# Kernel tuning notes

Measured on AMD Instinct MI355X. Metric: run time of the kernel, lower is better.

## Reference

```python
import jax, jax.numpy as jnp
import numpy as np

VOCAB = 32000
D_MODEL = 1024
PATCH_LEN = 16
NHEAD = 8
B = 8
S = 4096


def setup_inputs() -> dict:
    key = jax.random.key(0)
    ks = jax.random.split(key, 8)
    token_inputs = jax.random.randint(ks[0], (B, S), 0, VOCAB, dtype=jnp.int64 if jax.config.jax_enable_x64 else jnp.int32)
    attention_mask = jax.random.randint(ks[1], (B, S), 0, 2).astype(bool)
    emb_weight = jax.random.normal(ks[2], (VOCAB, D_MODEL), dtype=jnp.float32) * 0.02
    patch_query = jax.random.normal(ks[3], (1, 1, D_MODEL), dtype=jnp.float32) * 0.02
    # nn.MultiheadAttention packed in-projection [3D, D] and out projection [D, D]
    lim = 1.0 / np.sqrt(D_MODEL)
    in_proj_w = jax.random.uniform(ks[4], (3 * D_MODEL, D_MODEL), jnp.float32, -lim, lim)
    in_proj_b = jnp.zeros((3 * D_MODEL,), jnp.float32)
    out_w = jax.random.uniform(ks[5], (D_MODEL, D_MODEL), jnp.float32, -lim, lim)
    out_b = jnp.zeros((D_MODEL,), jnp.float32)
    return {
        "token_inputs": token_inputs,
        "attention_mask": attention_mask,
        "emb_weight": emb_weight,
        "patch_query": patch_query,
        "in_proj_w": in_proj_w,
        "in_proj_b": in_proj_b,
        "out_w": out_w,
        "out_b": out_b,
    }


def reference(token_inputs, attention_mask, emb_weight, patch_query, in_proj_w, in_proj_b, out_w, out_b):
    d_model = emb_weight.shape[1]
    h, dh = NHEAD, d_model // NHEAD
    L = PATCH_LEN

    tok_emb = emb_weight[token_inputs]              # [B, S, D]
    bsz, seqlen, _ = tok_emb.shape
    # seqlen chosen divisible by PATCH_LEN -> pad_len == 0 (matches torch path)
    num_patches = seqlen // L
    BP = bsz * num_patches
    patch_tokens = tok_emb.reshape(BP, L, d_model)  # [BP, L, D]
    patch_mask = attention_mask.reshape(BP, L)      # True = valid token

    patch_valid = patch_mask.any(axis=1)            # [BP]
    # force position 0 valid for fully-empty patches (safe softmax)
    safe_mask = patch_mask | ((~patch_valid)[:, None] & (jnp.arange(L) == 0)[None, :])

    wq, wk, wv = jnp.split(in_proj_w, 3, axis=0)    # each [D, D]
    bq, bk, bv = jnp.split(in_proj_b, 3, axis=0)

    q = patch_query[0, 0] @ wq.T + bq               # [D] (same query for all patches)
    k = patch_tokens @ wk.T + bk                    # [BP, L, D]
    v = patch_tokens @ wv.T + bv                    # [BP, L, D]

    qh = q.reshape(h, dh)                           # [H, dh]
    kh = k.reshape(BP, L, h, dh)                    # [BP, L, H, dh]
    vh = v.reshape(BP, L, h, dh)

    scale = 1.0 / jnp.sqrt(jnp.asarray(dh, q.dtype))
    scores = jnp.einsum('hd,blhd->bhl', qh, kh) * scale   # [BP, H, L]
    scores = jnp.where(safe_mask[:, None, :], scores, -jnp.inf)
    attn = jax.nn.softmax(scores, axis=-1)                # [BP, H, L]

    ctx = jnp.einsum('bhl,blhd->bhd', attn, vh).reshape(BP, d_model)
    patch_latent = ctx @ out_w.T + out_b                  # [BP, D]

    patch_latent = patch_latent.reshape(bsz, num_patches, d_model)
    pv = patch_valid.reshape(bsz, num_patches)
    patch_latent = patch_latent * pv[..., None].astype(patch_latent.dtype)
    return patch_latent, pv
```

## Files before the change

### kernel.cpp

```cpp
#include <hip/hip_runtime.h>
#include <stdint.h>

#define OUT_LATENT (2048*1024)
#define SCALE 0.08838834764831845f

typedef float f32x4v __attribute__((ext_vector_type(4)));
typedef short s16x8  __attribute__((ext_vector_type(8)));

static __device__ inline unsigned short f2bf(float f) {
    union { float f; uint32_t u; } v; v.f = f;
    uint32_t u = v.u;
    return (unsigned short)((u + 0x7FFFu + ((u >> 16) & 1u)) >> 16);
}
static __device__ inline float bflo(uint32_t u) {
    union { uint32_t u; float f; } v; v.u = u << 16; return v.f;
}
static __device__ inline float bfhi(uint32_t u) {
    union { uint32_t u; float f; } v; v.u = u & 0xFFFF0000u; return v.f;
}

static __device__ __forceinline__ void async16(const unsigned short* g, unsigned short* l) {
    __builtin_amdgcn_global_load_lds(
        (const __attribute__((address_space(1))) void*)g,
        (__attribute__((address_space(3))) void*)l, 16, 0, 0);
}

__global__ __launch_bounds__(256) void k_prep(
    const float* __restrict__ ipw, const float* __restrict__ ipb,
    const float* __restrict__ pq, const float* __restrict__ ow,
    unsigned short* __restrict__ wv_dst, unsigned short* __restrict__ ow_dst,
    unsigned short* __restrict__ qkb, float* __restrict__ sb) {
    __shared__ float qs[128];
    __shared__ float part[128];
    int t = threadIdx.x, b = blockIdx.x;

    if (b < 2048) {
        const float* src; unsigned short* dst; int idx;
        if (b < 1024) { src = ipw + (size_t)2048 * 1024; dst = wv_dst; idx = b * 1024 + t * 4; }
        else          { src = ow;                        dst = ow_dst; idx = (b - 1024) * 1024 + t * 4; }
        float4 f = *(const float4*)(src + idx);
        ushort4 o; o.x = f2bf(f.x); o.y = f2bf(f.y); o.z = f2bf(f.z); o.w = f2bf(f.w);
        *(ushort4*)(dst + idx) = o;
        return;
    }

    int bb = b - 2048;
    int h = bb >> 3, jseg = bb & 7;

    {
        int dl = t >> 1, half = t & 1;
        const float* wrow = ipw + (size_t)(h * 128 + dl) * 1024 + half * 512;
        const float* pqh = pq + half * 512;
        float a = 0.f;
        #pragma unroll 8
        for (int j = 0; j < 512; j += 4) {
            float4 w = *(const float4*)(wrow + j);
            float4 p = *(const float4*)(pqh + j);
            a = fmaf(w.x, p.x, a); a = fmaf(w.y, p.y, a);
            a = fmaf(w.z, p.z, a); a = fmaf(w.w, p.w, a);
        }
        a += __shfl_xor(a, 1);
        if (!half) qs[dl] = a + ipb[h * 128 + dl];
    }
    __syncthreads();

    int jl = t & 127, dh = t >> 7;
    float acc = 0.f;
    const float* wbase = ipw + (size_t)(1024 + h * 128 + dh * 64) * 1024 + jseg * 128 + jl;
    #pragma unroll 8
    for (int d = 0; d < 64; ++d)
        acc = fmaf(qs[dh * 64 + d], wbase[(size_t)d * 1024], acc);
    if (dh) part[jl] = acc;
    __syncthreads();
    if (!dh) qkb[h * 1024 + jseg * 128 + jl] = f2bf((acc + part[jl]) * SCALE);
    if (jseg == 0 && t < 64) {
        const float* bk = ipb + 1024 + h * 128;
        float p = qs[t] * bk[t] + qs[t + 64] * bk[t + 64];
        #pragma unroll
        for (int m = 32; m >= 1; m >>= 1) p += __shfl_xor(p, m);
        if (t == 0) sb[h] = p * SCALE;
    }
}

__global__ __launch_bounds__(256) void k_attn(
    const int* __restrict__ tok_ids, const int* __restrict__ amask,
    const float* __restrict__ emb, const unsigned short* __restrict__ qkb,
    const float* __restrict__ sb, unsigned short* __restrict__ Mout,
    float* __restrict__ pv) {
    __shared__ unsigned short tokL[16][1032];
    __shared__ float scoresP[4][16][8];
    __shared__ float attnL[16][8];
    __shared__ int allzL;

    int bp = blockIdx.x, t = threadIdx.x;
    int wave = t >> 6, lane = t & 63, lrow = lane & 15, quad = lane >> 4;

    s16x8 bfr[8];
    {
        const unsigned short* qbase = qkb + (lane & 7) * 1024 + wave * 256 + quad * 8;
        #pragma unroll
        for (int s = 0; s < 8; ++s) bfr[s] = *(const s16x8*)(qbase + s * 32);
    }

    {
        int row = t >> 4, c = t & 15;
        int tid = tok_ids[bp * 16 + row];
        const float* erow = emb + (size_t)tid * 1024;
        #pragma unroll
        for (int i = 0; i < 16; ++i) {
            int j4 = c + i * 16;
            float4 f = *(const float4*)(erow + j4 * 4);
            ushort4 o; o.x = f2bf(f.x); o.y = f2bf(f.y); o.z = f2bf(f.z); o.w = f2bf(f.w);
            *(ushort4*)(&tokL[row][j4 * 4]) = o;
        }
    }
    if (t < 16) {
        int any = (amask[bp * 16 + t] != 0);
        any |= __shfl_xor(any, 1); any |= __shfl_xor(any, 2);
        any |= __shfl_xor(any, 4); any |= __shfl_xor(any, 8);
        if (t == 0) { pv[bp] = any ? 1.f : 0.f; allzL = any ? 0 : 1; }
    }
    __syncthreads();

    {
        f32x4v acc = (f32x4v){0.f, 0.f, 0.f, 0.f};
        const unsigned short* arow = &tokL[lrow][wave * 256 + quad * 8];
        #pragma unroll
        for (int s = 0; s < 8; ++s) {
            s16x8 af = *(const s16x8*)(arow + s * 32);
            acc = __builtin_amdgcn_mfma_f32_16x16x32_bf16(af, bfr[s], acc, 0, 0, 0);
        }
        if (lrow < 8) {
            #pragma unroll
            for (int r = 0; r < 4; ++r) scoresP[wave][quad * 4 + r][lrow] = acc[r];
        }
    }
    __syncthreads();

    if (t < 128) {
        int hh = t >> 4, ll = t & 15;
        float s = scoresP[0][ll][hh] + scoresP[1][ll][hh]
                + scoresP[2][ll][hh] + scoresP[3][ll][hh] + sb[hh];
        bool valid = (amask[bp * 16 + ll] != 0) || (allzL && ll == 0);
        s = valid ? s : -1e30f;
        float mx = s;
        mx = fmaxf(mx, __shfl_xor(mx, 1)); mx = fmaxf(mx, __shfl_xor(mx, 2));
        mx = fmaxf(mx, __shfl_xor(mx, 4)); mx = fmaxf(mx, __shfl_xor(mx, 8));
        float e = __expf(s - mx);
        float sum = e;
        sum += __shfl_xor(sum, 1); sum += __shfl_xor(sum, 2);
        sum += __shfl_xor(sum, 4); sum += __shfl_xor(sum, 8);
        attnL[ll][hh] = e / sum;
    }
    __syncthreads();

    float macc[8][4];
    #pragma unroll
    for (int h = 0; h < 8; ++h)
        #pragma unroll
        for (int c = 0; c < 4; ++c) macc[h][c] = 0.f;
    #pragma unroll
    for (int ll = 0; ll < 16; ++ll) {
        uint2 tv = *(const uint2*)(&tokL[ll][t * 4]);
        float t0 = bflo(tv.x), t1 = bfhi(tv.x), t2 = bflo(tv.y), t3 = bfhi(tv.y);
        float4 a0 = *(const float4*)(&attnL[ll][0]);
        float4 a1 = *(const float4*)(&attnL[ll][4]);
        macc[0][0] = fmaf(a0.x, t0, macc[0][0]); macc[0][1] = fmaf(a0.x, t1, macc[0][1]);
        macc[0][2] = fmaf(a0.x, t2, macc[0][2]); macc[0][3] = fmaf(a0.x, t3, macc[0][3]);
        macc[1][0] = fmaf(a0.y, t0, macc[1][0]); macc[1][1] = fmaf(a0.y, t1, macc[1][1]);
        macc[1][2] = fmaf(a0.y, t2, macc[1][2]); macc[1][3] = fmaf(a0.y, t3, macc[1][3]);
        macc[2][0] = fmaf(a0.z, t0, macc[2][0]); macc[2][1] = fmaf(a0.z, t1, macc[2][1]);
        macc[2][2] = fmaf(a0.z, t2, macc[2][2]); macc[2][3] = fmaf(a0.z, t3, macc[2][3]);
        macc[3][0] = fmaf(a0.w, t0, macc[3][0]); macc[3][1] = fmaf(a0.w, t1, macc[3][1]);
        macc[3][2] = fmaf(a0.w, t2, macc[3][2]); macc[3][3] = fmaf(a0.w, t3, macc[3][3]);
        macc[4][0] = fmaf(a1.x, t0, macc[4][0]); macc[4][1] = fmaf(a1.x, t1, macc[4][1]);
        macc[4][2] = fmaf(a1.x, t2, macc[4][2]); macc[4][3] = fmaf(a1.x, t3, macc[4][3]);
        macc[5][0] = fmaf(a1.y, t0, macc[5][0]); macc[5][1] = fmaf(a1.y, t1, macc[5][1]);
        macc[5][2] = fmaf(a1.y, t2, macc[5][2]); macc[5][3] = fmaf(a1.y, t3, macc[5][3]);
        macc[6][0] = fmaf(a1.z, t0, macc[6][0]); macc[6][1] = fmaf(a1.z, t1, macc[6][1]);
        macc[6][2] = fmaf(a1.z, t2, macc[6][2]); macc[6][3] = fmaf(a1.z, t3, macc[6][3]);
        macc[7][0] = fmaf(a1.w, t0, macc[7][0]); macc[7][1] = fmaf(a1.w, t1, macc[7][1]);
        macc[7][2] = fmaf(a1.w, t2, macc[7][2]); macc[7][3] = fmaf(a1.w, t3, macc[7][3]);
    }
    #pragma unroll
    for (int h = 0; h < 8; ++h) {
        ushort4 o;
        o.x = f2bf(macc[h][0]); o.y = f2bf(macc[h][1]);
        o.z = f2bf(macc[h][2]); o.w = f2bf(macc[h][3]);
        *(ushort4*)(Mout + ((size_t)(h * 2048 + bp)) * 1024 + t * 4) = o;
    }
}

__device__ __forceinline__ void gemm64x128_dbuf(
    const unsigned short* __restrict__ A, const unsigned short* __restrict__ B,
    unsigned short* As, unsigned short* Bs, f32x4v acc[4][2]) {
    int t = threadIdx.x;
    int wave = t >> 6, lane = t & 63, lrow = lane & 15, quad = lane >> 4;
    int r4 = t >> 2, seg = (t & 3) * 8;
    #pragma unroll
    for (int mi = 0; mi < 4; ++mi)
        #pragma unroll
        for (int ni = 0; ni < 2; ++ni) acc[mi][ni] = (f32x4v){0.f, 0.f, 0.f, 0.f};
    async16(A + (size_t)r4 * 1024 + seg,        As + t * 8);
    async16(B + (size_t)r4 * 1024 + seg,        Bs + t * 8);
    async16(B + (size_t)(r4 + 64) * 1024 + seg, Bs + (256 + t) * 8);
    for (int s = 0; s < 32; ++s) {
        __syncthreads();
        if (s < 31) {
            int nk = (s + 1) * 32;
            int pb = (s + 1) & 1;
            async16(A + (size_t)r4 * 1024 + nk + seg,        As + pb * 2048 + t * 8);
            async16(B + (size_t)r4 * 1024 + nk + seg,        Bs + pb * 4096 + t * 8);
            async16(B + (size_t)(r4 + 64) * 1024 + nk + seg, Bs + pb * 4096 + (256 + t) * 8);
        }
        const unsigned short* Asc = As + (s & 1) * 2048;
        const unsigned short* Bsc = Bs + (s & 1) * 4096;
        s16x8 af[4], bf[2];
        #pragma unroll
        for (int mi = 0; mi < 4; ++mi)
            af[mi] = *(const s16x8*)(Asc + (mi * 16 + lrow) * 32 + quad * 8);
        #pragma unroll
        for (int ni = 0; ni < 2; ++ni)
            bf[ni] = *(const s16x8*)(Bsc + (wave * 32 + ni * 16 + lrow) * 32 + quad * 8);
        #pragma unroll
        for (int mi = 0; mi < 4; ++mi)
            #pragma unroll
            for (int ni = 0; ni < 2; ++ni)
                acc[mi][ni] = __builtin_amdgcn_mfma_f32_16x16x32_bf16(af[mi], bf[ni], acc[mi][ni], 0, 0, 0);
    }
}

__global__ __launch_bounds__(256) void k_gemm_ctx(
    const unsigned short* __restrict__ M, const unsigned short* __restrict__ wv,
    const float* __restrict__ ipb, unsigned short* __restrict__ ctx) {
    __shared__ unsigned short As[2 * 2048], Bs[2 * 4096];
    int mb = blockIdx.x, h = blockIdx.y;
    f32x4v acc[4][2];
    gemm64x128_dbuf(M + ((size_t)h * 2048 + mb * 64) * 1024,
                    wv + (size_t)h * 128 * 1024, As, Bs, acc);
    int t = threadIdx.x, wave = t >> 6, lane = t & 63, lrow = lane & 15, quad = lane >> 4;
    #pragma unroll
    for (int ni = 0; ni < 2; ++ni) {
        int n_g = h * 128 + wave * 32 + ni * 16 + lrow;
        float bias = ipb[2048 + n_g];
        #pragma unroll
        for (int mi = 0; mi < 4; ++mi) {
            #pragma unroll
            for (int r = 0; r < 4; ++r) {
                int m_g = mb * 64 + mi * 16 + quad * 4 + r;
                ctx[(size_t)m_g * 1024 + n_g] = f2bf(acc[mi][ni][r] + bias);
            }
        }
    }
}

__global__ __launch_bounds__(256) void k_gemm_out(
    const unsigned short* __restrict__ ctx, const unsigned short* __restrict__ ow,
    const float* __restrict__ outb, const float* __restrict__ pv,
    float* __restrict__ out) {
    __shared__ unsigned short As[2 * 2048], Bs[2 * 4096];
    int mb = blockIdx.x, nb = blockIdx.y;
    f32x4v acc[4][2];
    gemm64x128_dbuf(ctx + (size_t)mb * 64 * 1024,
                    ow + (size_t)nb * 128 * 1024, As, Bs, acc);
    int t = threadIdx.x, wave = t >> 6, lane = t & 63, lrow = lane & 15, quad = lane >> 4;
    #pragma unroll
    for (int ni = 0; ni < 2; ++ni) {
        int n_g = nb * 128 + wave * 32 + ni * 16 + lrow;
        float bias = outb[n_g];
        #pragma unroll
        for (int mi = 0; mi < 4; ++mi) {
            #pragma unroll
            for (int r = 0; r < 4; ++r) {
                int m_g = mb * 64 + mi * 16 + quad * 4 + r;
                out[(size_t)m_g * 1024 + n_g] = (acc[mi][ni][r] + bias) * pv[m_g];
            }
        }
    }
    if (nb == 0 && t < 64) out[OUT_LATENT + mb * 64 + t] = pv[mb * 64 + t];
}

extern "C" void kernel_launch(void* const* d_in, const int* in_sizes, int n_in,
                              void* d_out, int out_size, void* d_ws, size_t ws_size,
                              hipStream_t stream) {
    const int*   tok = (const int*)d_in[0];
    const int*   msk = (const int*)d_in[1];
    const float* emb = (const float*)d_in[2];
    const float* pq  = (const float*)d_in[3];
    const float* ipw = (const float*)d_in[4];
    const float* ipb = (const float*)d_in[5];
    const float* ow  = (const float*)d_in[6];
    const float* ob  = (const float*)d_in[7];
    float* out = (float*)d_out;
    char* ws = (char*)d_ws;

    float*          sb_f  = (float*)(ws + 4096);
    float*          pv_f  = (float*)(ws + 8192);
    unsigned short* qk_b  = (unsigned short*)(ws + 16384);
    unsigned short* wv_b  = (unsigned short*)(ws + 32768);
    unsigned short* ow_b  = (unsigned short*)(ws + 32768 + 2097152);
    unsigned short* ctx_b = (unsigned short*)(ws + 32768 + 2 * 2097152);
    unsigned short* M_b   = (unsigned short*)(ws + 32768 + 2 * 2097152 + 4194304);

    k_prep<<<dim3(2112), dim3(256), 0, stream>>>(ipw, ipb, pq, ow, wv_b, ow_b, qk_b, sb_f);
    k_attn<<<dim3(2048), dim3(256), 0, stream>>>(tok, msk, emb, qk_b, sb_f, M_b, pv_f);
    k_gemm_ctx<<<dim3(32, 8), dim3(256), 0, stream>>>(M_b, wv_b, ipb, ctx_b);
    k_gemm_out<<<dim3(32, 8), dim3(256), 0, stream>>>(ctx_b, ow_b, ob, pv_f, out);
}
```

Before: 300.6 us.

## Fuse all stages into a persistent megakernel with dependency counters

Replaces the four kernel launches with one persistent kernel where blocks pull work tickets from an atomic counter. Per-stage completion counters let the ctx and out GEMM tiles for one 128-row group start as soon as that group's attention and weight conversion finish, so stages overlap instead of serialising. GEMM tiles change from a double-buffered 64x128 tile to a single-buffered 128x64 tile, and shared memory becomes a union across roles. This adds spin-wait latency, per-step sync stalls from dropping double buffering, and a memset launch, and it relies on ticket order to avoid deadlock.

```diff
diff --git a/kernel.cpp b/kernel.cpp
--- a/kernel.cpp
+++ b/kernel.cpp
@@ -1,16 +1,23 @@
 #include <hip/hip_runtime.h>
 #include <stdint.h>
 
+typedef unsigned int u32;
+typedef unsigned short u16;
+
 #define OUT_LATENT (2048*1024)
 #define SCALE 0.08838834764831845f
 
 typedef float f32x4v __attribute__((ext_vector_type(4)));
 typedef short s16x8  __attribute__((ext_vector_type(8)));
 
-static __device__ inline unsigned short f2bf(float f) {
+#define T_CONV0 64
+#define T_G0    2112
+#define T_END   4672
+
+static __device__ inline u16 f2bf(float f) {
     union { float f; uint32_t u; } v; v.f = f;
     uint32_t u = v.u;
-    return (unsigned short)((u + 0x7FFFu + ((u >> 16) & 1u)) >> 16);
+    return (u16)((u + 0x7FFFu + ((u >> 16) & 1u)) >> 16);
 }
 static __device__ inline float bflo(uint32_t u) {
     union { uint32_t u; float f; } v; v.u = u << 16; return v.f;
@@ -18,35 +25,37 @@
 static __device__ inline float bfhi(uint32_t u) {
     union { uint32_t u; float f; } v; v.u = u & 0xFFFF0000u; return v.f;
 }
-
-static __device__ __forceinline__ void async16(const unsigned short* g, unsigned short* l) {
+static __device__ __forceinline__ void async16(const u16* g, u16* l) {
     __builtin_amdgcn_global_load_lds(
         (const __attribute__((address_space(1))) void*)g,
         (__attribute__((address_space(3))) void*)l, 16, 0, 0);
 }
 
-__global__ __launch_bounds__(256) void k_prep(
+union SMem {
+    struct { u16 tokL[16][1032]; float scoresP[4][16][8]; float attnL[16][8]; int allz; } a;
+    struct { u16 As[128 * 32]; u16 Bs[64 * 32]; } g;
+    struct { float qs[128]; float part[128]; } q;
+};
+
+static __device__ __forceinline__ void wait_ge(u32* p, u32 need) {
+    if (threadIdx.x == 0) {
+        while (__hip_atomic_load(p, __ATOMIC_RELAXED, __HIP_MEMORY_SCOPE_AGENT) < need)
+            __builtin_amdgcn_s_sleep(32);
+        (void)__hip_atomic_load(p, __ATOMIC_ACQUIRE, __HIP_MEMORY_SCOPE_AGENT);
+    }
+    __syncthreads();
+}
+static __device__ __forceinline__ void done_add(u32* p) {
+    __syncthreads();
+    if (threadIdx.x == 0)
+        (void)__hip_atomic_fetch_add(p, 1u, __ATOMIC_RELEASE, __HIP_MEMORY_SCOPE_AGENT);
+}
+
+static __device__ void role_qk(SMem& sm, int tk,
     const float* __restrict__ ipw, const float* __restrict__ ipb,
-    const float* __restrict__ pq, const float* __restrict__ ow,
-    unsigned short* __restrict__ wv_dst, unsigned short* __restrict__ ow_dst,
-    unsigned short* __restrict__ qkb, float* __restrict__ sb) {
-    __shared__ float qs[128];
-    __shared__ float part[128];
-    int t = threadIdx.x, b = blockIdx.x;
-
-    if (b < 2048) {
-        const float* src; unsigned short* dst; int idx;
-        if (b < 1024) { src = ipw + (size_t)2048 * 1024; dst = wv_dst; idx = b * 1024 + t * 4; }
-        else          { src = ow;                        dst = ow_dst; idx = (b - 1024) * 1024 + t * 4; }
-        float4 f = *(const float4*)(src + idx);
-        ushort4 o; o.x = f2bf(f.x); o.y = f2bf(f.y); o.z = f2bf(f.z); o.w = f2bf(f.w);
-        *(ushort4*)(dst + idx) = o;
-        return;
-    }
-
-    int bb = b - 2048;
-    int h = bb >> 3, jseg = bb & 7;
-
+    const float* __restrict__ pq, u16* __restrict__ qkb, float* __restrict__ sb,
+    u32* ctr) {
+    int h = tk >> 3, jseg = tk & 7, t = threadIdx.x;
     {
         int dl = t >> 1, half = t & 1;
         const float* wrow = ipw + (size_t)(h * 128 + dl) * 1024 + half * 512;
@@ -60,48 +69,55 @@
             a = fmaf(w.z, p.z, a); a = fmaf(w.w, p.w, a);
         }
         a += __shfl_xor(a, 1);
-        if (!half) qs[dl] = a + ipb[h * 128 + dl];
-    }
-    __syncthreads();
-
+        if (!half) sm.q.qs[dl] = a + ipb[h * 128 + dl];
+    }
+    __syncthreads();
     int jl = t & 127, dh = t >> 7;
     float acc = 0.f;
     const float* wbase = ipw + (size_t)(1024 + h * 128 + dh * 64) * 1024 + jseg * 128 + jl;
     #pragma unroll 8
     for (int d = 0; d < 64; ++d)
-        acc = fmaf(qs[dh * 64 + d], wbase[(size_t)d * 1024], acc);
-    if (dh) part[jl] = acc;
-    __syncthreads();
-    if (!dh) qkb[h * 1024 + jseg * 128 + jl] = f2bf((acc + part[jl]) * SCALE);
+        acc = fmaf(sm.q.qs[dh * 64 + d], wbase[(size_t)d * 1024], acc);
+    if (dh) sm.q.part[jl] = acc;
+    __syncthreads();
+    if (!dh) qkb[h * 1024 + jseg * 128 + jl] = f2bf((acc + sm.q.part[jl]) * SCALE);
     if (jseg == 0 && t < 64) {
         const float* bk = ipb + 1024 + h * 128;
-        float p = qs[t] * bk[t] + qs[t + 64] * bk[t + 64];
+        float p = sm.q.qs[t] * bk[t] + sm.q.qs[t + 64] * bk[t + 64];
         #pragma unroll
         for (int m = 32; m >= 1; m >>= 1) p += __shfl_xor(p, m);
         if (t == 0) sb[h] = p * SCALE;
     }
-}
-
-__global__ __launch_bounds__(256) void k_attn(
+    done_add(ctr + 1);
+}
+
+static __device__ void role_conv(int b,
+    const float* __restrict__ ipw, const float* __restrict__ ow,
+    u16* __restrict__ wv_dst, u16* __restrict__ ow_dst, u32* ctr) {
+    int t = threadIdx.x;
+    const float* src; u16* dst; int idx;
+    if (b < 1024) { src = ipw + (size_t)2048 * 1024; dst = wv_dst; idx = b * 1024 + t * 4; }
+    else          { src = ow;                        dst = ow_dst; idx = (b - 1024) * 1024 + t * 4; }
+    float4 f = *(const float4*)(src + idx);
+    ushort4 o; o.x = f2bf(f.x); o.y = f2bf(f.y); o.z = f2bf(f.z); o.w = f2bf(f.w);
+    *(ushort4*)(dst + idx) = o;
+    done_add(ctr + (b < 1024 ? 2 : 3));
+}
+
+static __device__ void role_attn(SMem& sm, int bp,
     const int* __restrict__ tok_ids, const int* __restrict__ amask,
-    const float* __restrict__ emb, const unsigned short* __restrict__ qkb,
-    const float* __restrict__ sb, unsigned short* __restrict__ Mout,
-    float* __restrict__ pv) {
-    __shared__ unsigned short tokL[16][1032];
-    __shared__ float scoresP[4][16][8];
-    __shared__ float attnL[16][8];
-    __shared__ int allzL;
-
-    int bp = blockIdx.x, t = threadIdx.x;
+    const float* __restrict__ emb, const u16* __restrict__ qkb,
+    const float* __restrict__ sb, u16* __restrict__ Mout,
+    float* __restrict__ pv, u32* ctr) {
+    int t = threadIdx.x;
     int wave = t >> 6, lane = t & 63, lrow = lane & 15, quad = lane >> 4;
 
     s16x8 bfr[8];
     {
-        const unsigned short* qbase = qkb + (lane & 7) * 1024 + wave * 256 + quad * 8;
+        const u16* qbase = qkb + (lane & 7) * 1024 + wave * 256 + quad * 8;
         #pragma unroll
         for (int s = 0; s < 8; ++s) bfr[s] = *(const s16x8*)(qbase + s * 32);
     }
-
     {
         int row = t >> 4, c = t & 15;
         int tid = tok_ids[bp * 16 + row];
@@ -111,20 +127,20 @@
             int j4 = c + i * 16;
             float4 f = *(const float4*)(erow + j4 * 4);
             ushort4 o; o.x = f2bf(f.x); o.y = f2bf(f.y); o.z = f2bf(f.z); o.w = f2bf(f.w);
-            *(ushort4*)(&tokL[row][j4 * 4]) = o;
+            *(ushort4*)(&sm.a.tokL[row][j4 * 4]) = o;
         }
     }
     if (t < 16) {
         int any = (amask[bp * 16 + t] != 0);
         any |= __shfl_xor(any, 1); any |= __shfl_xor(any, 2);
         any |= __shfl_xor(any, 4); any |= __shfl_xor(any, 8);
-        if (t == 0) { pv[bp] = any ? 1.f : 0.f; allzL = any ? 0 : 1; }
+        if (t == 0) { pv[bp] = any ? 1.f : 0.f; sm.a.allz = any ? 0 : 1; }
     }
     __syncthreads();
 
     {
         f32x4v acc = (f32x4v){0.f, 0.f, 0.f, 0.f};
-        const unsigned short* arow = &tokL[lrow][wave * 256 + quad * 8];
+        const u16* arow = &sm.a.tokL[lrow][wave * 256 + quad * 8];
         #pragma unroll
         for (int s = 0; s < 8; ++s) {
             s16x8 af = *(const s16x8*)(arow + s * 32);
@@ -132,16 +148,16 @@
         }
         if (lrow < 8) {
             #pragma unroll
-            for (int r = 0; r < 4; ++r) scoresP[wave][quad * 4 + r][lrow] = acc[r];
+            for (int r = 0; r < 4; ++r) sm.a.scoresP[wave][quad * 4 + r][lrow] = acc[r];
         }
     }
     __syncthreads();
 
     if (t < 128) {
         int hh = t >> 4, ll = t & 15;
-        float s = scoresP[0][ll][hh] + scoresP[1][ll][hh]
-                + scoresP[2][ll][hh] + scoresP[3][ll][hh] + sb[hh];
-        bool valid = (amask[bp * 16 + ll] != 0) || (allzL && ll == 0);
+        float s = sm.a.scoresP[0][ll][hh] + sm.a.scoresP[1][ll][hh]
+                + sm.a.scoresP[2][ll][hh] + sm.a.scoresP[3][ll][hh] + sb[hh];
+        bool valid = (amask[bp * 16 + ll] != 0) || (sm.a.allz && ll == 0);
         s = valid ? s : -1e30f;
         float mx = s;
         mx = fmaxf(mx, __shfl_xor(mx, 1)); mx = fmaxf(mx, __shfl_xor(mx, 2));
@@ -150,7 +166,7 @@
         float sum = e;
         sum += __shfl_xor(sum, 1); sum += __shfl_xor(sum, 2);
         sum += __shfl_xor(sum, 4); sum += __shfl_xor(sum, 8);
-        attnL[ll][hh] = e / sum;
+        sm.a.attnL[ll][hh] = e / sum;
     }
     __syncthreads();
 
@@ -161,10 +177,10 @@
         for (int c = 0; c < 4; ++c) macc[h][c] = 0.f;
     #pragma unroll
     for (int ll = 0; ll < 16; ++ll) {
-        uint2 tv = *(const uint2*)(&tokL[ll][t * 4]);
+        uint2 tv = *(const uint2*)(&sm.a.tokL[ll][t * 4]);
         float t0 = bflo(tv.x), t1 = bfhi(tv.x), t2 = bflo(tv.y), t3 = bfhi(tv.y);
-        float4 a0 = *(const float4*)(&attnL[ll][0]);
-        float4 a1 = *(const float4*)(&attnL[ll][4]);
+        float4 a0 = *(const float4*)(&sm.a.attnL[ll][0]);
+        float4 a1 = *(const float4*)(&sm.a.attnL[ll][4]);
         macc[0][0] = fmaf(a0.x, t0, macc[0][0]); macc[0][1] = fmaf(a0.x, t1, macc[0][1]);
         macc[0][2] = fmaf(a0.x, t2, macc[0][2]); macc[0][3] = fmaf(a0.x, t3, macc[0][3]);
         macc[1][0] = fmaf(a0.y, t0, macc[1][0]); macc[1][1] = fmaf(a0.y, t1, macc[1][1]);
@@ -189,39 +205,35 @@
         o.z = f2bf(macc[h][2]); o.w = f2bf(macc[h][3]);
         *(ushort4*)(Mout + ((size_t)(h * 2048 + bp)) * 1024 + t * 4) = o;
     }
-}
-
-__device__ __forceinline__ void gemm64x128_dbuf(
-    const unsigned short* __restrict__ A, const unsigned short* __restrict__ B,
-    unsigned short* As, unsigned short* Bs, f32x4v acc[4][2]) {
+    done_add(ctr + 4 + (bp >> 7));
+}
+
+static __device__ __forceinline__ void gemm_tile_128x64(
+    const u16* __restrict__ A, const u16* __restrict__ B, SMem& sm,
+    f32x4v acc[4][2]) {
     int t = threadIdx.x;
     int wave = t >> 6, lane = t & 63, lrow = lane & 15, quad = lane >> 4;
+    int wm = wave & 1, wn = wave >> 1;
     int r4 = t >> 2, seg = (t & 3) * 8;
+    u16* As = sm.g.As; u16* Bs = sm.g.Bs;
     #pragma unroll
     for (int mi = 0; mi < 4; ++mi)
         #pragma unroll
         for (int ni = 0; ni < 2; ++ni) acc[mi][ni] = (f32x4v){0.f, 0.f, 0.f, 0.f};
-    async16(A + (size_t)r4 * 1024 + seg,        As + t * 8);
-    async16(B + (size_t)r4 * 1024 + seg,        Bs + t * 8);
-    async16(B + (size_t)(r4 + 64) * 1024 + seg, Bs + (256 + t) * 8);
-    for (int s = 0; s < 32; ++s) {
+    for (int step = 0; step < 32; ++step) {
+        int k0 = step * 32;
         __syncthreads();
-        if (s < 31) {
-            int nk = (s + 1) * 32;
-            int pb = (s + 1) & 1;
-            async16(A + (size_t)r4 * 1024 + nk + seg,        As + pb * 2048 + t * 8);
-            async16(B + (size_t)r4 * 1024 + nk + seg,        Bs + pb * 4096 + t * 8);
-            async16(B + (size_t)(r4 + 64) * 1024 + nk + seg, Bs + pb * 4096 + (256 + t) * 8);
-        }
-        const unsigned short* Asc = As + (s & 1) * 2048;
-        const unsigned short* Bsc = Bs + (s & 1) * 4096;
+        async16(A + (size_t)r4 * 1024 + k0 + seg,        As + t * 8);
+        async16(A + (size_t)(r4 + 64) * 1024 + k0 + seg, As + (256 + t) * 8);
+        async16(B + (size_t)r4 * 1024 + k0 + seg,        Bs + t * 8);
+        __syncthreads();
         s16x8 af[4], bf[2];
         #pragma unroll
         for (int mi = 0; mi < 4; ++mi)
-            af[mi] = *(const s16x8*)(Asc + (mi * 16 + lrow) * 32 + quad * 8);
+            af[mi] = *(const s16x8*)(As + (wm * 64 + mi * 16 + lrow) * 32 + quad * 8);
         #pragma unroll
         for (int ni = 0; ni < 2; ++ni)
-            bf[ni] = *(const s16x8*)(Bsc + (wave * 32 + ni * 16 + lrow) * 32 + quad * 8);
+            bf[ni] = *(const s16x8*)(Bs + (wn * 32 + ni * 16 + lrow) * 32 + quad * 8);
         #pragma unroll
         for (int mi = 0; mi < 4; ++mi)
             #pragma unroll
@@ -230,54 +242,94 @@
     }
 }
 
-__global__ __launch_bounds__(256) void k_gemm_ctx(
-    const unsigned short* __restrict__ M, const unsigned short* __restrict__ wv,
-    const float* __restrict__ ipb, unsigned short* __restrict__ ctx) {
-    __shared__ unsigned short As[2 * 2048], Bs[2 * 4096];
-    int mb = blockIdx.x, h = blockIdx.y;
+static __device__ void role_ctx(SMem& sm, int mb, int cn,
+    const u16* __restrict__ M, const u16* __restrict__ wv,
+    const float* __restrict__ ipb, u16* __restrict__ ctx, u32* ctr) {
+    int h = cn >> 1;
     f32x4v acc[4][2];
-    gemm64x128_dbuf(M + ((size_t)h * 2048 + mb * 64) * 1024,
-                    wv + (size_t)h * 128 * 1024, As, Bs, acc);
+    gemm_tile_128x64(M + ((size_t)h * 2048 + mb * 128) * 1024,
+                     wv + (size_t)cn * 64 * 1024, sm, acc);
     int t = threadIdx.x, wave = t >> 6, lane = t & 63, lrow = lane & 15, quad = lane >> 4;
+    int wm = wave & 1, wn = wave >> 1;
     #pragma unroll
     for (int ni = 0; ni < 2; ++ni) {
-        int n_g = h * 128 + wave * 32 + ni * 16 + lrow;
+        int n_g = cn * 64 + wn * 32 + ni * 16 + lrow;
         float bias = ipb[2048 + n_g];
         #pragma unroll
         for (int mi = 0; mi < 4; ++mi) {
             #pragma unroll
             for (int r = 0; r < 4; ++r) {
-                int m_g = mb * 64 + mi * 16 + quad * 4 + r;
+                int m_g = mb * 128 + wm * 64 + mi * 16 + quad * 4 + r;
                 ctx[(size_t)m_g * 1024 + n_g] = f2bf(acc[mi][ni][r] + bias);
             }
         }
     }
-}
-
-__global__ __launch_bounds__(256) void k_gemm_out(
-    const unsigned short* __restrict__ ctx, const unsigned short* __restrict__ ow,
+    done_add(ctr + 20 + mb);
+}
+
+static __device__ void role_out(SMem& sm, int mb, int nt,
+    const u16* __restrict__ ctx, const u16* __restrict__ ow,
     const float* __restrict__ outb, const float* __restrict__ pv,
     float* __restrict__ out) {
-    __shared__ unsigned short As[2 * 2048], Bs[2 * 4096];
-    int mb = blockIdx.x, nb = blockIdx.y;
     f32x4v acc[4][2];
-    gemm64x128_dbuf(ctx + (size_t)mb * 64 * 1024,
-                    ow + (size_t)nb * 128 * 1024, As, Bs, acc);
+    gemm_tile_128x64(ctx + (size_t)mb * 128 * 1024,
+                     ow + (size_t)nt * 64 * 1024, sm, acc);
     int t = threadIdx.x, wave = t >> 6, lane = t & 63, lrow = lane & 15, quad = lane >> 4;
+    int wm = wave & 1, wn = wave >> 1;
     #pragma unroll
     for (int ni = 0; ni < 2; ++ni) {
-        int n_g = nb * 128 + wave * 32 + ni * 16 + lrow;
+        int n_g = nt * 64 + wn * 32 + ni * 16 + lrow;
         float bias = outb[n_g];
         #pragma unroll
         for (int mi = 0; mi < 4; ++mi) {
             #pragma unroll
             for (int r = 0; r < 4; ++r) {
-                int m_g = mb * 64 + mi * 16 + quad * 4 + r;
+                int m_g = mb * 128 + wm * 64 + mi * 16 + quad * 4 + r;
                 out[(size_t)m_g * 1024 + n_g] = (acc[mi][ni][r] + bias) * pv[m_g];
             }
         }
     }
-    if (nb == 0 && t < 64) out[OUT_LATENT + mb * 64 + t] = pv[mb * 64 + t];
+    if (nt == 0 && t < 128) out[OUT_LATENT + mb * 128 + t] = pv[mb * 128 + t];
+}
+
+__global__ __launch_bounds__(256, 4) void k_mega(
+    const int* __restrict__ tok, const int* __restrict__ msk,
+    const float* __restrict__ emb, const float* __restrict__ pq,
+    const float* __restrict__ ipw, const float* __restrict__ ipb,
+    const float* __restrict__ ow, const float* __restrict__ ob,
+    float* __restrict__ out, u32* ctr, float* sb, float* pv,
+    u16* qkb, u16* wv_b, u16* ow_b, u16* ctx_b, u16* M_b) {
+    __shared__ SMem sm;
+    __shared__ u32 tkS;
+    bool qk_ok = false, wv_ok = false, ow_ok = false;
+    for (;;) {
+        __syncthreads();
+        if (threadIdx.x == 0)
+            tkS = __hip_atomic_fetch_add(ctr, 1u, __ATOMIC_RELAXED, __HIP_MEMORY_SCOPE_AGENT);
+        __syncthreads();
+        u32 tk = tkS;
+        if (tk >= T_END) return;
+        if (tk < T_CONV0) {
+            role_qk(sm, tk, ipw, ipb, pq, qkb, sb, ctr);
+        } else if (tk < T_G0) {
+            role_conv(tk - T_CONV0, ipw, ow, wv_b, ow_b, ctr);
+        } else {
+            u32 r = tk - T_G0;
+            u32 g = r / 160u, o = r % 160u;
+            if (o < 128) {
+                if (!qk_ok) { wait_ge(ctr + 1, 64); qk_ok = true; }
+                role_attn(sm, g * 128 + o, tok, msk, emb, qkb, sb, M_b, pv, ctr);
+            } else if (o < 144) {
+                if (!wv_ok) { wait_ge(ctr + 2, 1024); wv_ok = true; }
+                wait_ge(ctr + 4 + g, 128);
+                role_ctx(sm, g, o - 128, M_b, wv_b, ipb, ctx_b, ctr);
+            } else {
+                if (!ow_ok) { wait_ge(ctr + 3, 1024); ow_ok = true; }
+                wait_ge(ctr + 20 + g, 16);
+                role_out(sm, g, o - 144, ctx_b, ow_b, ob, pv, out);
+            }
+        }
+    }
 }
 
 extern "C" void kernel_launch(void* const* d_in, const int* in_sizes, int n_in,
@@ -294,16 +346,17 @@
     float* out = (float*)d_out;
     char* ws = (char*)d_ws;
 
-    float*          sb_f  = (float*)(ws + 4096);
-    float*          pv_f  = (float*)(ws + 8192);
-    unsigned short* qk_b  = (unsigned short*)(ws + 16384);
-    unsigned short* wv_b  = (unsigned short*)(ws + 32768);
-    unsigned short* ow_b  = (unsigned short*)(ws + 32768 + 2097152);
-    unsigned short* ctx_b = (unsigned short*)(ws + 32768 + 2 * 2097152);
-    unsigned short* M_b   = (unsigned short*)(ws + 32768 + 2 * 2097152 + 4194304);
-
-    k_prep<<<dim3(2112), dim3(256), 0, stream>>>(ipw, ipb, pq, ow, wv_b, ow_b, qk_b, sb_f);
-    k_attn<<<dim3(2048), dim3(256), 0, stream>>>(tok, msk, emb, qk_b, sb_f, M_b, pv_f);
-    k_gemm_ctx<<<dim3(32, 8), dim3(256), 0, stream>>>(M_b, wv_b, ipb, ctx_b);
-    k_gemm_out<<<dim3(32, 8), dim3(256), 0, stream>>>(ctx_b, ow_b, ob, pv_f, out);
-}
+    u32*   ctr   = (u32*)(ws + 0);
+    float* sb_f  = (float*)(ws + 4096);
+    float* pv_f  = (float*)(ws + 8192);
+    u16*   qk_b  = (u16*)(ws + 16384);
+    u16*   wv_b  = (u16*)(ws + 32768);
+    u16*   ow_b  = (u16*)(ws + 32768 + 2097152);
+    u16*   ctx_b = (u16*)(ws + 32768 + 2 * 2097152);
+    u16*   M_b   = (u16*)(ws + 32768 + 2 * 2097152 + 4194304);
+
+    hipMemsetAsync(ws, 0, 256, stream);
+    k_mega<<<dim3(1024), dim3(256), 0, stream>>>(
+        tok, msk, emb, pq, ipw, ipb, ow, ob, out,
+        ctr, sb_f, pv_f, qk_b, wv_b, ow_b, ctx_b, M_b);
+}
```

Result: slower. 882.2 us (+193.5%).

## Enlarge GEMM tiles to 128x128 with BK64 swizzled LDS and batch embedding loads

Applied to the files above, without the earlier changes.

Both GEMMs move from 64x128 double-buffered tiles with BK32 to 128x128 tiles with BK64, using an XOR swizzle on the LDS layout to avoid bank conflicts and a 2x2 wave arrangement for more operand reuse per MFMA. Double buffering is dropped in favour of sync-load-sync per step, so global loads no longer overlap compute. The grid halves to 128 blocks per GEMM, which leaves many CUs idle on a 256-CU part. The attention kernel also issues its embedding row loads in batches of eight before converting, to raise memory-level parallelism.

```diff
diff --git a/kernel.cpp b/kernel.cpp
--- a/kernel.cpp
+++ b/kernel.cpp
@@ -1,16 +1,18 @@
 #include <hip/hip_runtime.h>
 #include <stdint.h>
 
+typedef unsigned short u16;
+
 #define OUT_LATENT (2048*1024)
 #define SCALE 0.08838834764831845f
 
 typedef float f32x4v __attribute__((ext_vector_type(4)));
 typedef short s16x8  __attribute__((ext_vector_type(8)));
 
-static __device__ inline unsigned short f2bf(float f) {
+static __device__ inline u16 f2bf(float f) {
     union { float f; uint32_t u; } v; v.f = f;
     uint32_t u = v.u;
-    return (unsigned short)((u + 0x7FFFu + ((u >> 16) & 1u)) >> 16);
+    return (u16)((u + 0x7FFFu + ((u >> 16) & 1u)) >> 16);
 }
 static __device__ inline float bflo(uint32_t u) {
     union { uint32_t u; float f; } v; v.u = u << 16; return v.f;
@@ -18,8 +20,7 @@
 static __device__ inline float bfhi(uint32_t u) {
     union { uint32_t u; float f; } v; v.u = u & 0xFFFF0000u; return v.f;
 }
-
-static __device__ __forceinline__ void async16(const unsigned short* g, unsigned short* l) {
+static __device__ __forceinline__ void async16(const u16* g, u16* l) {
     __builtin_amdgcn_global_load_lds(
         (const __attribute__((address_space(1))) void*)g,
         (__attribute__((address_space(3))) void*)l, 16, 0, 0);
@@ -28,14 +29,14 @@
 __global__ __launch_bounds__(256) void k_prep(
     const float* __restrict__ ipw, const float* __restrict__ ipb,
     const float* __restrict__ pq, const float* __restrict__ ow,
-    unsigned short* __restrict__ wv_dst, unsigned short* __restrict__ ow_dst,
-    unsigned short* __restrict__ qkb, float* __restrict__ sb) {
+    u16* __restrict__ wv_dst, u16* __restrict__ ow_dst,
+    u16* __restrict__ qkb, float* __restrict__ sb) {
     __shared__ float qs[128];
     __shared__ float part[128];
     int t = threadIdx.x, b = blockIdx.x;
 
     if (b < 2048) {
-        const float* src; unsigned short* dst; int idx;
+        const float* src; u16* dst; int idx;
         if (b < 1024) { src = ipw + (size_t)2048 * 1024; dst = wv_dst; idx = b * 1024 + t * 4; }
         else          { src = ow;                        dst = ow_dst; idx = (b - 1024) * 1024 + t * 4; }
         float4 f = *(const float4*)(src + idx);
@@ -46,7 +47,6 @@
 
     int bb = b - 2048;
     int h = bb >> 3, jseg = bb & 7;
-
     {
         int dl = t >> 1, half = t & 1;
         const float* wrow = ipw + (size_t)(h * 128 + dl) * 1024 + half * 512;
@@ -63,7 +63,6 @@
         if (!half) qs[dl] = a + ipb[h * 128 + dl];
     }
     __syncthreads();
-
     int jl = t & 127, dh = t >> 7;
     float acc = 0.f;
     const float* wbase = ipw + (size_t)(1024 + h * 128 + dh * 64) * 1024 + jseg * 128 + jl;
@@ -84,10 +83,10 @@
 
 __global__ __launch_bounds__(256) void k_attn(
     const int* __restrict__ tok_ids, const int* __restrict__ amask,
-    const float* __restrict__ emb, const unsigned short* __restrict__ qkb,
-    const float* __restrict__ sb, unsigned short* __restrict__ Mout,
+    const float* __restrict__ emb, const u16* __restrict__ qkb,
+    const float* __restrict__ sb, u16* __restrict__ Mout,
     float* __restrict__ pv) {
-    __shared__ unsigned short tokL[16][1032];
+    __shared__ u16 tokL[16][1032];
     __shared__ float scoresP[4][16][8];
     __shared__ float attnL[16][8];
     __shared__ int allzL;
@@ -95,36 +94,45 @@
     int bp = blockIdx.x, t = threadIdx.x;
     int wave = t >> 6, lane = t & 63, lrow = lane & 15, quad = lane >> 4;
 
-    s16x8 bfr[8];
-    {
-        const unsigned short* qbase = qkb + (lane & 7) * 1024 + wave * 256 + quad * 8;
-        #pragma unroll
-        for (int s = 0; s < 8; ++s) bfr[s] = *(const s16x8*)(qbase + s * 32);
-    }
-
-    {
-        int row = t >> 4, c = t & 15;
-        int tid = tok_ids[bp * 16 + row];
-        const float* erow = emb + (size_t)tid * 1024;
-        #pragma unroll
-        for (int i = 0; i < 16; ++i) {
-            int j4 = c + i * 16;
-            float4 f = *(const float4*)(erow + j4 * 4);
-            ushort4 o; o.x = f2bf(f.x); o.y = f2bf(f.y); o.z = f2bf(f.z); o.w = f2bf(f.w);
-            *(ushort4*)(&tokL[row][j4 * 4]) = o;
-        }
-    }
     if (t < 16) {
         int any = (amask[bp * 16 + t] != 0);
         any |= __shfl_xor(any, 1); any |= __shfl_xor(any, 2);
         any |= __shfl_xor(any, 4); any |= __shfl_xor(any, 8);
         if (t == 0) { pv[bp] = any ? 1.f : 0.f; allzL = any ? 0 : 1; }
     }
+
+    int row = t >> 4, c = t & 15;
+    int tid = tok_ids[bp * 16 + row];
+    const float* erow = emb + (size_t)tid * 1024;
+    float4 ld[8];
+    #pragma unroll
+    for (int i = 0; i < 8; ++i) ld[i] = *(const float4*)(erow + (c + i * 16) * 4);
+
+    s16x8 bfr[8];
+    {
+        const u16* qbase = qkb + (lane & 7) * 1024 + wave * 256 + quad * 8;
+        #pragma unroll
+        for (int s = 0; s < 8; ++s) bfr[s] = *(const s16x8*)(qbase + s * 32);
+    }
+    #pragma unroll
+    for (int i = 0; i < 8; ++i) {
+        ushort4 o; o.x = f2bf(ld[i].x); o.y = f2bf(ld[i].y);
+        o.z = f2bf(ld[i].z); o.w = f2bf(ld[i].w);
+        *(ushort4*)(&tokL[row][(c + i * 16) * 4]) = o;
+    }
+    #pragma unroll
+    for (int i = 0; i < 8; ++i) ld[i] = *(const float4*)(erow + (c + (i + 8) * 16) * 4);
+    #pragma unroll
+    for (int i = 0; i < 8; ++i) {
+        ushort4 o; o.x = f2bf(ld[i].x); o.y = f2bf(ld[i].y);
+        o.z = f2bf(ld[i].z); o.w = f2bf(ld[i].w);
+        *(ushort4*)(&tokL[row][(c + (i + 8) * 16) * 4]) = o;
+    }
     __syncthreads();
 
     {
         f32x4v acc = (f32x4v){0.f, 0.f, 0.f, 0.f};
-        const unsigned short* arow = &tokL[lrow][wave * 256 + quad * 8];
+        const u16* arow = &tokL[lrow][wave * 256 + quad * 8];
         #pragma unroll
         for (int s = 0; s < 8; ++s) {
             s16x8 af = *(const s16x8*)(arow + s * 32);
@@ -158,7 +166,7 @@
     #pragma unroll
     for (int h = 0; h < 8; ++h)
         #pragma unroll
-        for (int c = 0; c < 4; ++c) macc[h][c] = 0.f;
+        for (int cc = 0; cc < 4; ++cc) macc[h][cc] = 0.f;
     #pragma unroll
     for (int ll = 0; ll < 16; ++ll) {
         uint2 tv = *(const uint2*)(&tokL[ll][t * 4]);
@@ -191,63 +199,66 @@
     }
 }
 
-__device__ __forceinline__ void gemm64x128_dbuf(
-    const unsigned short* __restrict__ A, const unsigned short* __restrict__ B,
-    unsigned short* As, unsigned short* Bs, f32x4v acc[4][2]) {
+__device__ __forceinline__ void gemm128_bk64(
+    const u16* __restrict__ A, const u16* __restrict__ B,
+    u16* As, u16* Bs, f32x4v acc[4][4]) {
     int t = threadIdx.x;
     int wave = t >> 6, lane = t & 63, lrow = lane & 15, quad = lane >> 4;
-    int r4 = t >> 2, seg = (t & 3) * 8;
+    int wm = wave & 1, wn = wave >> 1;
+    int tr = t >> 3, tc7 = t & 7;
     #pragma unroll
     for (int mi = 0; mi < 4; ++mi)
         #pragma unroll
-        for (int ni = 0; ni < 2; ++ni) acc[mi][ni] = (f32x4v){0.f, 0.f, 0.f, 0.f};
-    async16(A + (size_t)r4 * 1024 + seg,        As + t * 8);
-    async16(B + (size_t)r4 * 1024 + seg,        Bs + t * 8);
-    async16(B + (size_t)(r4 + 64) * 1024 + seg, Bs + (256 + t) * 8);
-    for (int s = 0; s < 32; ++s) {
+        for (int ni = 0; ni < 4; ++ni) acc[mi][ni] = (f32x4v){0.f, 0.f, 0.f, 0.f};
+    for (int step = 0; step < 16; ++step) {
+        int k0 = step * 64;
         __syncthreads();
-        if (s < 31) {
-            int nk = (s + 1) * 32;
-            int pb = (s + 1) & 1;
-            async16(A + (size_t)r4 * 1024 + nk + seg,        As + pb * 2048 + t * 8);
-            async16(B + (size_t)r4 * 1024 + nk + seg,        Bs + pb * 4096 + t * 8);
-            async16(B + (size_t)(r4 + 64) * 1024 + nk + seg, Bs + pb * 4096 + (256 + t) * 8);
-        }
-        const unsigned short* Asc = As + (s & 1) * 2048;
-        const unsigned short* Bsc = Bs + (s & 1) * 4096;
-        s16x8 af[4], bf[2];
-        #pragma unroll
-        for (int mi = 0; mi < 4; ++mi)
-            af[mi] = *(const s16x8*)(Asc + (mi * 16 + lrow) * 32 + quad * 8);
-        #pragma unroll
-        for (int ni = 0; ni < 2; ++ni)
-            bf[ni] = *(const s16x8*)(Bsc + (wave * 32 + ni * 16 + lrow) * 32 + quad * 8);
-        #pragma unroll
-        for (int mi = 0; mi < 4; ++mi)
-            #pragma unroll
-            for (int ni = 0; ni < 2; ++ni)
-                acc[mi][ni] = __builtin_amdgcn_mfma_f32_16x16x32_bf16(af[mi], bf[ni], acc[mi][ni], 0, 0, 0);
+        #pragma unroll
+        for (int rb = 0; rb < 128; rb += 32) {
+            int r = rb + tr;
+            int gofs = (tc7 ^ (r & 7)) * 8;
+            async16(A + (size_t)r * 1024 + k0 + gofs, As + rb * 64 + t * 8);
+            async16(B + (size_t)r * 1024 + k0 + gofs, Bs + rb * 64 + t * 8);
+        }
+        __syncthreads();
+        #pragma unroll
+        for (int kk = 0; kk < 2; ++kk) {
+            s16x8 af[4], bf[4];
+            #pragma unroll
+            for (int i = 0; i < 4; ++i) {
+                int ra = wm * 64 + i * 16 + lrow;
+                af[i] = *(const s16x8*)(As + ra * 64 + (((kk * 4 + quad) ^ (ra & 7)) * 8));
+                int rb2 = wn * 64 + i * 16 + lrow;
+                bf[i] = *(const s16x8*)(Bs + rb2 * 64 + (((kk * 4 + quad) ^ (rb2 & 7)) * 8));
+            }
+            #pragma unroll
+            for (int mi = 0; mi < 4; ++mi)
+                #pragma unroll
+                for (int ni = 0; ni < 4; ++ni)
+                    acc[mi][ni] = __builtin_amdgcn_mfma_f32_16x16x32_bf16(af[mi], bf[ni], acc[mi][ni], 0, 0, 0);
+        }
     }
 }
 
 __global__ __launch_bounds__(256) void k_gemm_ctx(
-    const unsigned short* __restrict__ M, const unsigned short* __restrict__ wv,
-    const float* __restrict__ ipb, unsigned short* __restrict__ ctx) {
-    __shared__ unsigned short As[2 * 2048], Bs[2 * 4096];
+    const u16* __restrict__ M, const u16* __restrict__ wv,
+    const float* __restrict__ ipb, u16* __restrict__ ctx) {
+    __shared__ u16 As[128 * 64], Bs[128 * 64];
     int mb = blockIdx.x, h = blockIdx.y;
-    f32x4v acc[4][2];
-    gemm64x128_dbuf(M + ((size_t)h * 2048 + mb * 64) * 1024,
-                    wv + (size_t)h * 128 * 1024, As, Bs, acc);
+    f32x4v acc[4][4];
+    gemm128_bk64(M + ((size_t)h * 2048 + mb * 128) * 1024,
+                 wv + (size_t)h * 128 * 1024, As, Bs, acc);
     int t = threadIdx.x, wave = t >> 6, lane = t & 63, lrow = lane & 15, quad = lane >> 4;
-    #pragma unroll
-    for (int ni = 0; ni < 2; ++ni) {
-        int n_g = h * 128 + wave * 32 + ni * 16 + lrow;
+    int wm = wave & 1, wn = wave >> 1;
+    #pragma unroll
+    for (int ni = 0; ni < 4; ++ni) {
+        int n_g = h * 128 + wn * 64 + ni * 16 + lrow;
         float bias = ipb[2048 + n_g];
         #pragma unroll
         for (int mi = 0; mi < 4; ++mi) {
             #pragma unroll
             for (int r = 0; r < 4; ++r) {
-                int m_g = mb * 64 + mi * 16 + quad * 4 + r;
+                int m_g = mb * 128 + wm * 64 + mi * 16 + quad * 4 + r;
                 ctx[(size_t)m_g * 1024 + n_g] = f2bf(acc[mi][ni][r] + bias);
             }
         }
@@ -255,29 +266,30 @@
 }
 
 __global__ __launch_bounds__(256) void k_gemm_out(
-    const unsigned short* __restrict__ ctx, const unsigned short* __restrict__ ow,
+    const u16* __restrict__ ctx, const u16* __restrict__ ow,
     const float* __restrict__ outb, const float* __restrict__ pv,
     float* __restrict__ out) {
-    __shared__ unsigned short As[2 * 2048], Bs[2 * 4096];
+    __shared__ u16 As[128 * 64], Bs[128 * 64];
     int mb = blockIdx.x, nb = blockIdx.y;
-    f32x4v acc[4][2];
-    gemm64x128_dbuf(ctx + (size_t)mb * 64 * 1024,
-                    ow + (size_t)nb * 128 * 1024, As, Bs, acc);
+    f32x4v acc[4][4];
+    gemm128_bk64(ctx + (size_t)mb * 128 * 1024,
+                 ow + (size_t)nb * 128 * 1024, As, Bs, acc);
     int t = threadIdx.x, wave = t >> 6, lane = t & 63, lrow = lane & 15, quad = lane >> 4;
-    #pragma unroll
-    for (int ni = 0; ni < 2; ++ni) {
-        int n_g = nb * 128 + wave * 32 + ni * 16 + lrow;
+    int wm = wave & 1, wn = wave >> 1;
+    #pragma unroll
+    for (int ni = 0; ni < 4; ++ni) {
+        int n_g = nb * 128 + wn * 64 + ni * 16 + lrow;
         float bias = outb[n_g];
         #pragma unroll
         for (int mi = 0; mi < 4; ++mi) {
             #pragma unroll
             for (int r = 0; r < 4; ++r) {
-                int m_g = mb * 64 + mi * 16 + quad * 4 + r;
+                int m_g = mb * 128 + wm * 64 + mi * 16 + quad * 4 + r;
                 out[(size_t)m_g * 1024 + n_g] = (acc[mi][ni][r] + bias) * pv[m_g];
             }
         }
     }
-    if (nb == 0 && t < 64) out[OUT_LATENT + mb * 64 + t] = pv[mb * 64 + t];
+    if (nb == 0 && t < 128) out[OUT_LATENT + mb * 128 + t] = pv[mb * 128 + t];
 }
 
 extern "C" void kernel_launch(void* const* d_in, const int* in_sizes, int n_in,
@@ -294,16 +306,16 @@
     float* out = (float*)d_out;
     char* ws = (char*)d_ws;
 
-    float*          sb_f  = (float*)(ws + 4096);
-    float*          pv_f  = (float*)(ws + 8192);
-    unsigned short* qk_b  = (unsigned short*)(ws + 16384);
-    unsigned short* wv_b  = (unsigned short*)(ws + 32768);
-    unsigned short* ow_b  = (unsigned short*)(ws + 32768 + 2097152);
-    unsigned short* ctx_b = (unsigned short*)(ws + 32768 + 2 * 2097152);
-    unsigned short* M_b   = (unsigned short*)(ws + 32768 + 2 * 2097152 + 4194304);
+    float* sb_f  = (float*)(ws + 4096);
+    float* pv_f  = (float*)(ws + 8192);
+    u16*   qk_b  = (u16*)(ws + 16384);
+    u16*   wv_b  = (u16*)(ws + 32768);
+    u16*   ow_b  = (u16*)(ws + 32768 + 2097152);
+    u16*   ctx_b = (u16*)(ws + 32768 + 2 * 2097152);
+    u16*   M_b   = (u16*)(ws + 32768 + 2 * 2097152 + 4194304);
 
     k_prep<<<dim3(2112), dim3(256), 0, stream>>>(ipw, ipb, pq, ow, wv_b, ow_b, qk_b, sb_f);
     k_attn<<<dim3(2048), dim3(256), 0, stream>>>(tok, msk, emb, qk_b, sb_f, M_b, pv_f);
-    k_gemm_ctx<<<dim3(32, 8), dim3(256), 0, stream>>>(M_b, wv_b, ipb, ctx_b);
-    k_gemm_out<<<dim3(32, 8), dim3(256), 0, stream>>>(ctx_b, ow_b, ob, pv_f, out);
-}
+    k_gemm_ctx<<<dim3(16, 8), dim3(256), 0, stream>>>(M_b, wv_b, ipb, ctx_b);
+    k_gemm_out<<<dim3(16, 8), dim3(256), 0, stream>>>(ctx_b, ow_b, ob, pv_f, out);
+}
```

Measured after the change: 299.1 us. About the same (-0.5%).
